# Kernel optimization log

Hardware: AMD Instinct MI355X
Metric: run time of the kernel (lower is better)

The kernel has to match this reference:

```python
import jax, jax.numpy as jnp
import numpy as np

G = 60            # 60x60 macroblock MV grid (960px / 16px blocks)
IMAGE_SIZE = 960.0
LN_EPS = 1e-5


def layer_norm(x, g, b):
    mu = jnp.mean(x, -1, keepdims=True)
    var = jnp.var(x, -1, keepdims=True)
    return (x - mu) / jnp.sqrt(var + LN_EPS) * g + b


def setup_inputs() -> dict:
    key = jax.random.key(0)
    ks = iter(jax.random.split(key, 40))
    nk = lambda: next(ks)
    N = 4096
    MVF, BED, H = 64, 32, 128
    D_IN = MVF + BED  # 96

    def lin(out_d, in_d):
        w = jax.random.normal(nk(), (out_d, in_d), jnp.float32) * np.float32(1.0 / np.sqrt(in_d))
        b = jnp.zeros((out_d,), jnp.float32)
        return w, b

    motion_vectors = jax.random.normal(nk(), (1, 2, G, G), jnp.float32)
    xy = jax.random.uniform(nk(), (N, 2), jnp.float32, 0.0, 800.0)
    wh = jax.random.uniform(nk(), (N, 2), jnp.float32, 16.0, 160.0)
    boxes = jnp.concatenate([xy, jnp.clip(xy + wh, 0.0, IMAGE_SIZE)], axis=-1)

    inp = {"motion_vectors": motion_vectors, "boxes": boxes}
    # stats projection: 6 stats (mean/std/range x 2 channels) -> MVF
    inp["W_stats"], inp["b_stats"] = lin(MVF, 6)
    inp["g_stats"] = jnp.ones((MVF,), jnp.float32); inp["be_stats"] = jnp.zeros((MVF,), jnp.float32)
    # box coordinate encoder
    inp["W_b1"], inp["b_b1"] = lin(BED, 4)
    inp["g_b1"] = jnp.ones((BED,), jnp.float32); inp["be_b1"] = jnp.zeros((BED,), jnp.float32)
    inp["W_b2"], inp["b_b2"] = lin(BED, BED)
    inp["g_b2"] = jnp.ones((BED,), jnp.float32); inp["be_b2"] = jnp.zeros((BED,), jnp.float32)
    # single-layer LSTM (torch gate order i,f,g,o)
    inp["W_ih"] = jax.random.normal(nk(), (4 * H, D_IN), jnp.float32) * np.float32(1.0 / np.sqrt(D_IN))
    inp["W_hh"] = jax.random.normal(nk(), (4 * H, H), jnp.float32) * np.float32(1.0 / np.sqrt(H))
    inp["b_ih"] = jnp.zeros((4 * H,), jnp.float32)
    inp["b_hh"] = jnp.zeros((4 * H,), jnp.float32)
    # heads
    inp["W_p1"], inp["b_p1"] = lin(H // 2, H); inp["W_p2"], inp["b_p2"] = lin(2, H // 2)
    inp["W_s1"], inp["b_s1"] = lin(H // 2, H); inp["W_s2"], inp["b_s2"] = lin(2, H // 2)
    inp["W_c1"], inp["b_c1"] = lin(H // 2, H); inp["W_c2"], inp["b_c2"] = lin(1, H // 2)
    return inp


def _box_motion_stats(motion_vectors, boxes_norm):
    # motion_vectors: [1,2,G,G]; boxes_norm: [N,4] in [0,1]
    mvf = motion_vectors[0].reshape(2, G * G)  # [2, 3600]
    x1 = jnp.clip(jnp.floor(boxes_norm[:, 0] * G).astype(jnp.int32), 0, G - 1)
    y1 = jnp.clip(jnp.floor(boxes_norm[:, 1] * G).astype(jnp.int32), 0, G - 1)
    x2 = jnp.clip(jnp.ceil(boxes_norm[:, 2] * G).astype(jnp.int32), x1 + 1, G)
    y2 = jnp.clip(jnp.ceil(boxes_norm[:, 3] * G).astype(jnp.int32), y1 + 1, G)
    idx = jnp.arange(G)
    mx = (idx[None, :] >= x1[:, None]) & (idx[None, :] < x2[:, None])  # [N,G]
    my = (idx[None, :] >= y1[:, None]) & (idx[None, :] < y2[:, None])  # [N,G]
    mask = (my[:, :, None] & mx[:, None, :]).reshape(-1, G * G).astype(mvf.dtype)  # [N,3600]
    cnt = mask.sum(-1, keepdims=True)  # >= 1 by construction
    s = jnp.einsum('nc,kc->nk', mask, mvf)          # [N,2]
    sq = jnp.einsum('nc,kc->nk', mask, mvf * mvf)   # [N,2]
    mean = s / cnt
    std = jnp.sqrt(jnp.clip(sq / cnt - mean * mean, 0.0))
    big = jnp.asarray(1e30, mvf.dtype)
    hi = jnp.where(mask[:, None, :] > 0, mvf[None], -big).max(-1)  # [N,2]
    lo = jnp.where(mask[:, None, :] > 0, mvf[None], big).min(-1)   # [N,2]
    return jnp.concatenate([mean, std, hi - lo], axis=-1)  # [N,6]


def reference(motion_vectors, boxes,
              W_stats, b_stats, g_stats, be_stats,
              W_b1, b_b1, g_b1, be_b1, W_b2, b_b2, g_b2, be_b2,
              W_ih, W_hh, b_ih, b_hh,
              W_p1, b_p1, W_p2, b_p2, W_s1, b_s1, W_s2, b_s2, W_c1, b_c1, W_c2, b_c2):
    N = boxes.shape[0]
    H = W_hh.shape[1]
    boxes_norm = jnp.clip(boxes / IMAGE_SIZE, 0.0, 1.0)

    # per-box motion feature (BoxAlignedMotionEncoder: gather region -> mean/std/range -> proj)
    stats = _box_motion_stats(motion_vectors, boxes_norm)
    mv_feat = jax.nn.relu(layer_norm(stats @ W_stats.T + b_stats, g_stats, be_stats))  # [N,64]

    # box coordinate encoder (dropout = identity in eval)
    h1 = jax.nn.relu(layer_norm(boxes_norm @ W_b1.T + b_b1, g_b1, be_b1))
    box_feat = jax.nn.relu(layer_norm(h1 @ W_b2.T + b_b2, g_b2, be_b2))  # [N,32]

    x = jnp.concatenate([mv_feat, box_feat], axis=-1)  # [N,96]

    # single-step LSTM, zero initial state, torch gate order i,f,g,o
    h0 = jnp.zeros((N, H), x.dtype)
    c0 = jnp.zeros((N, H), x.dtype)
    gates = x @ W_ih.T + h0 @ W_hh.T + b_ih + b_hh
    i, f, g, o = jnp.split(gates, 4, axis=-1)
    c = jax.nn.sigmoid(f) * c0 + jax.nn.sigmoid(i) * jnp.tanh(g)
    h = jax.nn.sigmoid(o) * jnp.tanh(c)  # [N,128]

    pos = jax.nn.relu(h @ W_p1.T + b_p1) @ W_p2.T + b_p2    # [N,2]
    size = jax.nn.relu(h @ W_s1.T + b_s1) @ W_s2.T + b_s2   # [N,2]
    conf = jax.nn.relu(h @ W_c1.T + b_c1) @ W_c2.T + b_c2   # [N,1]
    confidences = jax.nn.sigmoid(conf[:, 0])

    # box update: shift center by deltas, scale w/h by exp(size_deltas)
    x1, y1, x2, y2 = boxes[:, 0], boxes[:, 1], boxes[:, 2], boxes[:, 3]
    cx, cy = (x1 + x2) * 0.5, (y1 + y2) * 0.5
    w, hgt = x2 - x1, y2 - y1
    ncx, ncy = cx + pos[:, 0], cy + pos[:, 1]
    nw, nh = w * jnp.exp(size[:, 0]), hgt * jnp.exp(size[:, 1])
    pred = jnp.stack([ncx - nw * 0.5, ncy - nh * 0.5, ncx + nw * 0.5, ncy + nh * 0.5], axis=-1)
    return jnp.concatenate([pred, confidences[:, None]], axis=-1)  # [N,5]
```

## Files before the change

### kernel.cpp

```cpp
#include <hip/hip_runtime.h>
#include <math.h>

#define GRID_G 60
#define GRID_GG 3600
#define BPB 8

__device__ __forceinline__ float wred32sum(float v){
  #pragma unroll
  for (int m = 16; m; m >>= 1) v += __shfl_xor(v, m, 32);
  return v;
}
__device__ __forceinline__ float wred32max(float v){
  #pragma unroll
  for (int m = 16; m; m >>= 1) v = fmaxf(v, __shfl_xor(v, m, 32));
  return v;
}
__device__ __forceinline__ float wred32min(float v){
  #pragma unroll
  for (int m = 16; m; m >>= 1) v = fminf(v, __shfl_xor(v, m, 32));
  return v;
}
__device__ __forceinline__ float frcp(float x){ return __builtin_amdgcn_rcpf(x); }
__device__ __forceinline__ float fsig(float x){ return frcp(1.0f + __expf(-x)); }
__device__ __forceinline__ float ftanh(float x){ return 1.0f - 2.0f*frcp(1.0f + __expf(2.0f*x)); }

__device__ __forceinline__ unsigned short f2bf(float x){
  unsigned int u = __float_as_uint(x);
  return (unsigned short)((u + 0x7fffu + ((u >> 16) & 1u)) >> 16);
}
__device__ __forceinline__ float bf_lo(unsigned int u){ return __uint_as_float(u << 16); }
__device__ __forceinline__ float bf_hi(unsigned int u){ return __uint_as_float(u & 0xffff0000u); }

__global__ __launch_bounds__(256) void transpose_kernel(
    const float* __restrict__ W_ih,
    const float* __restrict__ W_p1, const float* __restrict__ W_s1,
    const float* __restrict__ W_c1,
    unsigned int* __restrict__ wt_ih2, unsigned int* __restrict__ wt_h2)
{
  const int i = blockIdx.x * 256 + threadIdx.x;
  if (i < 18432) {
    const int e = i * 2;
    const int k = e / 384, r0 = e % 384;
    const int row0 = (r0     < 128) ? r0     : r0 + 128;
    const int row1 = (r0 + 1 < 128) ? r0 + 1 : r0 + 1 + 128;
    const unsigned int lo = f2bf(W_ih[row0 * 96 + k]);
    const unsigned int hi = f2bf(W_ih[row1 * 96 + k]);
    wt_ih2[i] = lo | (hi << 16);
  } else if (i < 18432 + 12288) {
    const int j = i - 18432;
    const int e = j * 2;
    const int k = e / 192, r0 = e % 192;
    const float* W = (r0 < 64) ? W_p1 : (r0 < 128) ? W_s1 : W_c1;
    const unsigned int lo = f2bf(W[((r0    ) & 63) * 128 + k]);
    const unsigned int hi = f2bf(W[((r0 + 1) & 63) * 128 + k]);
    wt_h2[j] = lo | (hi << 16);
  }
}

__global__ __launch_bounds__(256) void tracker_kernel(
    const float* __restrict__ mv,
    const float* __restrict__ boxes,
    const float* __restrict__ W_stats, const float* __restrict__ b_stats,
    const float* __restrict__ g_stats, const float* __restrict__ be_stats,
    const float* __restrict__ W_b1,  const float* __restrict__ b_b1,
    const float* __restrict__ g_b1,  const float* __restrict__ be_b1,
    const float* __restrict__ W_b2,  const float* __restrict__ b_b2,
    const float* __restrict__ g_b2,  const float* __restrict__ be_b2,
    const unsigned int* __restrict__ wt_ih2,
    const float* __restrict__ b_ih,  const float* __restrict__ b_hh,
    const unsigned int* __restrict__ wt_h2,
    const float* __restrict__ b_p1,  const float* __restrict__ W_p2, const float* __restrict__ b_p2,
    const float* __restrict__ b_s1,  const float* __restrict__ W_s2, const float* __restrict__ b_s2,
    const float* __restrict__ b_c1,  const float* __restrict__ W_c2, const float* __restrict__ b_c2,
    float* __restrict__ out, int N)
{
  __shared__ __align__(16) float x_lds[BPB][96];
  __shared__ __align__(16) float sP[4][BPB][384];
  __shared__ __align__(16) float h_lds[BPB][128];
  __shared__ __align__(16) float h1_lds[BPB][32];
  __shared__ float u_lds[3*BPB][65];
  __shared__ float res_lds[BPB][5];

  const int tid  = threadIdx.x;
  const int base = blockIdx.x * BPB;

  {
    const int b   = tid >> 5;
    const int l32 = tid & 31;
    int gb = base + b; if (gb >= N) gb = N - 1;
    const float4 bx = ((const float4*)boxes)[gb];
    const float bn0 = fminf(fmaxf(bx.x * (1.0f/960.0f), 0.f), 1.f);
    const float bn1 = fminf(fmaxf(bx.y * (1.0f/960.0f), 0.f), 1.f);
    const float bn2 = fminf(fmaxf(bx.z * (1.0f/960.0f), 0.f), 1.f);
    const float bn3 = fminf(fmaxf(bx.w * (1.0f/960.0f), 0.f), 1.f);

    int x1 = (int)floorf(bn0 * 60.f); x1 = min(max(x1, 0), 59);
    int y1 = (int)floorf(bn1 * 60.f); y1 = min(max(y1, 0), 59);
    int x2 = (int)ceilf (bn2 * 60.f); x2 = min(max(x2, x1 + 1), 60);
    int y2 = (int)ceilf (bn3 * 60.f); y2 = min(max(y2, y1 + 1), 60);
    const int w = x2 - x1, hh = y2 - y1;
    const int cnt = w * hh;
    const float rw = 1.0f / (float)w;

    float s0=0.f, s1=0.f, q0=0.f, q1=0.f;
    float hi0=-1e30f, hi1=-1e30f, lo0=1e30f, lo1=1e30f;
    for (int c = l32; c < cnt; c += 32) {
      const int yy = (int)(((float)c + 0.5f) * rw);
      const int xx = c - yy * w;
      const int idx = (y1 + yy) * GRID_G + (x1 + xx);
      const float m0 = mv[idx];
      const float m1 = mv[GRID_GG + idx];
      s0 += m0; q0 += m0*m0; hi0 = fmaxf(hi0, m0); lo0 = fminf(lo0, m0);
      s1 += m1; q1 += m1*m1; hi1 = fmaxf(hi1, m1); lo1 = fminf(lo1, m1);
    }
    s0 = wred32sum(s0); q0 = wred32sum(q0); hi0 = wred32max(hi0); lo0 = wred32min(lo0);
    s1 = wred32sum(s1); q1 = wred32sum(q1); hi1 = wred32max(hi1); lo1 = wred32min(lo1);
    const float inv = frcp((float)cnt);
    float st[6];
    st[0] = s0 * inv;
    st[1] = s1 * inv;
    st[2] = sqrtf(fmaxf(q0 * inv - st[0]*st[0], 0.f));
    st[3] = sqrtf(fmaxf(q1 * inv - st[1]*st[1], 0.f));
    st[4] = hi0 - lo0;
    st[5] = hi1 - lo1;

    {
      const float* Wr0 = W_stats + l32 * 6;
      const float* Wr1 = W_stats + (l32 + 32) * 6;
      float v0 = b_stats[l32], v1 = b_stats[l32 + 32];
      #pragma unroll
      for (int k = 0; k < 6; ++k) { v0 = fmaf(st[k], Wr0[k], v0); v1 = fmaf(st[k], Wr1[k], v1); }
      const float mu  = wred32sum(v0 + v1) * (1.0f/64.0f);
      const float var = wred32sum(v0*v0 + v1*v1) * (1.0f/64.0f) - mu*mu;
      const float rs  = rsqrtf(var + 1e-5f);
      x_lds[b][l32     ] = fmaxf((v0-mu)*rs*g_stats[l32     ] + be_stats[l32     ], 0.f);
      x_lds[b][l32 + 32] = fmaxf((v1-mu)*rs*g_stats[l32 + 32] + be_stats[l32 + 32], 0.f);
    }

    {
      const float* Wr = W_b1 + l32 * 4;
      const float v = b_b1[l32] + bn0*Wr[0] + bn1*Wr[1] + bn2*Wr[2] + bn3*Wr[3];
      const float mu  = wred32sum(v)   * (1.0f/32.0f);
      const float var = wred32sum(v*v) * (1.0f/32.0f) - mu*mu;
      h1_lds[b][l32] = fmaxf((v - mu) * rsqrtf(var + 1e-5f) * g_b1[l32] + be_b1[l32], 0.f);
    }
    __threadfence_block();

    {
      const float* Wr = W_b2 + l32 * 32;
      float v = b_b2[l32];
      #pragma unroll
      for (int kk = 0; kk < 8; ++kk) {
        const float4 hv = *(const float4*)(&h1_lds[b][kk * 4]);
        const float4 wv = *(const float4*)(&Wr[kk * 4]);
        v = fmaf(wv.x,hv.x, fmaf(wv.y,hv.y, fmaf(wv.z,hv.z, fmaf(wv.w,hv.w, v))));
      }
      const float mu  = wred32sum(v)   * (1.0f/32.0f);
      const float var = wred32sum(v*v) * (1.0f/32.0f) - mu*mu;
      x_lds[b][64 + l32] = fmaxf((v - mu) * rsqrtf(var + 1e-5f) * g_b2[l32] + be_b2[l32], 0.f);
    }
  }
  __syncthreads();

  if (tid < 192) {
    const int o = tid % 48;
    const int s = tid / 48;
    const int k0 = s * 24;
    float acc[8][BPB];
    #pragma unroll
    for (int j = 0; j < 8; ++j)
      #pragma unroll
      for (int b = 0; b < BPB; ++b) acc[j][b] = 0.f;
    #pragma unroll 2
    for (int k4 = 0; k4 < 6; ++k4) {
      const int kb = k0 + 4*k4;
      uint4 W[4];
      #pragma unroll
      for (int kk = 0; kk < 4; ++kk)
        W[kk] = *(const uint4*)(wt_ih2 + ((size_t)(kb + kk) * 384 + 8*o) / 2);
      float4 xv[BPB];
      #pragma unroll
      for (int b = 0; b < BPB; ++b) xv[b] = *(const float4*)(&x_lds[b][kb]);
      #pragma unroll
      for (int kk = 0; kk < 4; ++kk) {
        const float w0 = bf_lo(W[kk].x), w1 = bf_hi(W[kk].x);
        const float w2 = bf_lo(W[kk].y), w3 = bf_hi(W[kk].y);
        const float w4 = bf_lo(W[kk].z), w5 = bf_hi(W[kk].z);
        const float w6 = bf_lo(W[kk].w), w7 = bf_hi(W[kk].w);
        #pragma unroll
        for (int b = 0; b < BPB; ++b) {
          const float xc = (kk == 0) ? xv[b].x : (kk == 1) ? xv[b].y : (kk == 2) ? xv[b].z : xv[b].w;
          acc[0][b] = fmaf(w0, xc, acc[0][b]);
          acc[1][b] = fmaf(w1, xc, acc[1][b]);
          acc[2][b] = fmaf(w2, xc, acc[2][b]);
          acc[3][b] = fmaf(w3, xc, acc[3][b]);
          acc[4][b] = fmaf(w4, xc, acc[4][b]);
          acc[5][b] = fmaf(w5, xc, acc[5][b]);
          acc[6][b] = fmaf(w6, xc, acc[6][b]);
          acc[7][b] = fmaf(w7, xc, acc[7][b]);
        }
      }
    }
    #pragma unroll
    for (int b = 0; b < BPB; ++b) {
      float4 v0; v0.x = acc[0][b]; v0.y = acc[1][b]; v0.z = acc[2][b]; v0.w = acc[3][b];
      float4 v1; v1.x = acc[4][b]; v1.y = acc[5][b]; v1.z = acc[6][b]; v1.w = acc[7][b];
      *(float4*)(&sP[s][b][8*o    ]) = v0;
      *(float4*)(&sP[s][b][8*o + 4]) = v1;
    }
  }
  __syncthreads();

  {
    const int j  = tid & 127;
    const int g2 = tid >> 7;
    const float bi = b_ih[j      ] + b_hh[j      ];
    const float bg = b_ih[j + 256] + b_hh[j + 256];
    const float bo = b_ih[j + 384] + b_hh[j + 384];
    #pragma unroll
    for (int bb = 0; bb < 4; ++bb) {
      const int b = g2 * 4 + bb;
      const float ai = sP[0][b][j      ] + sP[1][b][j      ] + sP[2][b][j      ] + sP[3][b][j      ] + bi;
      const float ag = sP[0][b][128 + j] + sP[1][b][128 + j] + sP[2][b][128 + j] + sP[3][b][128 + j] + bg;
      const float ao = sP[0][b][256 + j] + sP[1][b][256 + j] + sP[2][b][256 + j] + sP[3][b][256 + j] + bo;
      const float c  = fsig(ai) * ftanh(ag);
      h_lds[b][j] = fsig(ao) * ftanh(c);
    }
  }
  __syncthreads();

  if (tid < 192) {
    const int o  = tid % 24;
    const int s8 = tid / 24;
    const int k0 = s8 * 16;
    float acc[8][BPB];
    #pragma unroll
    for (int j = 0; j < 8; ++j)
      #pragma unroll
      for (int b = 0; b < BPB; ++b) acc[j][b] = 0.f;
    #pragma unroll 2
    for (int k4 = 0; k4 < 4; ++k4) {
      const int kb = k0 + 4*k4;
      uint4 W[4];
      #pragma unroll
      for (int kk = 0; kk < 4; ++kk)
        W[kk] = *(const uint4*)(wt_h2 + ((size_t)(kb + kk) * 192 + 8*o) / 2);
      float4 hv[BPB];
      #pragma unroll
      for (int b = 0; b < BPB; ++b) hv[b] = *(const float4*)(&h_lds[b][kb]);
      #pragma unroll
      for (int kk = 0; kk < 4; ++kk) {
        const float w0 = bf_lo(W[kk].x), w1 = bf_hi(W[kk].x);
        const float w2 = bf_lo(W[kk].y), w3 = bf_hi(W[kk].y);
        const float w4 = bf_lo(W[kk].z), w5 = bf_hi(W[kk].z);
        const float w6 = bf_lo(W[kk].w), w7 = bf_hi(W[kk].w);
        #pragma unroll
        for (int b = 0; b < BPB; ++b) {
          const float hc = (kk == 0) ? hv[b].x : (kk == 1) ? hv[b].y : (kk == 2) ? hv[b].z : hv[b].w;
          acc[0][b] = fmaf(w0, hc, acc[0][b]);
          acc[1][b] = fmaf(w1, hc, acc[1][b]);
          acc[2][b] = fmaf(w2, hc, acc[2][b]);
          acc[3][b] = fmaf(w3, hc, acc[3][b]);
          acc[4][b] = fmaf(w4, hc, acc[4][b]);
          acc[5][b] = fmaf(w5, hc, acc[5][b]);
          acc[6][b] = fmaf(w6, hc, acc[6][b]);
          acc[7][b] = fmaf(w7, hc, acc[7][b]);
        }
      }
    }
    const int buf = s8 >> 1;
    const int off = (s8 & 1) * 192;
    #pragma unroll
    for (int b = 0; b < BPB; ++b) {
      float4 v0; v0.x = acc[0][b]; v0.y = acc[1][b]; v0.z = acc[2][b]; v0.w = acc[3][b];
      float4 v1; v1.x = acc[4][b]; v1.y = acc[5][b]; v1.z = acc[6][b]; v1.w = acc[7][b];
      *(float4*)(&sP[buf][b][off + 8*o    ]) = v0;
      *(float4*)(&sP[buf][b][off + 8*o + 4]) = v1;
    }
  }
  __syncthreads();

  {
    #pragma unroll
    for (int i = 0; i < 6; ++i) {
      const int idx = tid + 256 * i;
      const int b = idx / 192;
      const int r = idx - b * 192;
      const int head = r >> 6, brow = r & 63;
      const float bias = ((head == 0) ? b_p1 : (head == 1) ? b_s1 : b_c1)[brow];
      float v = bias;
      #pragma unroll
      for (int p = 0; p < 8; ++p) v += sP[p >> 1][b][(p & 1) * 192 + r];
      u_lds[head * BPB + b][brow] = fmaxf(v, 0.f);
    }
  }
  __syncthreads();

  if (tid < BPB * 5) {
    const int b = tid / 5, o = tid % 5;
    const int head = (o < 2) ? 0 : (o < 4) ? 1 : 2;
    const float* W2; float bias;
    if      (o == 0) { W2 = W_p2;      bias = b_p2[0]; }
    else if (o == 1) { W2 = W_p2 + 64; bias = b_p2[1]; }
    else if (o == 2) { W2 = W_s2;      bias = b_s2[0]; }
    else if (o == 3) { W2 = W_s2 + 64; bias = b_s2[1]; }
    else             { W2 = W_c2;      bias = b_c2[0]; }
    const float* ur = u_lds[head * BPB + b];
    float a0 = bias, a1 = 0.f, a2 = 0.f, a3 = 0.f;
    #pragma unroll 4
    for (int k = 0; k < 64; k += 4) {
      a0 = fmaf(ur[k  ], W2[k  ], a0);
      a1 = fmaf(ur[k+1], W2[k+1], a1);
      a2 = fmaf(ur[k+2], W2[k+2], a2);
      a3 = fmaf(ur[k+3], W2[k+3], a3);
    }
    res_lds[b][o] = (a0 + a1) + (a2 + a3);
  }
  __syncthreads();

  if (tid < BPB) {
    const int gb = base + tid;
    if (gb < N) {
      const float4 bx = ((const float4*)boxes)[gb];
      const float cx = (bx.x + bx.z) * 0.5f;
      const float cy = (bx.y + bx.w) * 0.5f;
      const float w  = bx.z - bx.x;
      const float hh = bx.w - bx.y;
      const float ncx = cx + res_lds[tid][0];
      const float ncy = cy + res_lds[tid][1];
      const float nw  = w  * __expf(res_lds[tid][2]);
      const float nh  = hh * __expf(res_lds[tid][3]);
      const float cf  = fsig(res_lds[tid][4]);
      float* op = out + (size_t)gb * 5;
      op[0] = ncx - nw * 0.5f;
      op[1] = ncy - nh * 0.5f;
      op[2] = ncx + nw * 0.5f;
      op[3] = ncy + nh * 0.5f;
      op[4] = cf;
    }
  }
}

extern "C" void kernel_launch(void* const* d_in, const int* in_sizes, int n_in,
                              void* d_out, int out_size, void* d_ws, size_t ws_size,
                              hipStream_t stream) {
  (void)n_in; (void)out_size; (void)ws_size;
  const float* mv       = (const float*)d_in[0];
  const float* boxes    = (const float*)d_in[1];
  const float* W_stats  = (const float*)d_in[2];
  const float* b_stats  = (const float*)d_in[3];
  const float* g_stats  = (const float*)d_in[4];
  const float* be_stats = (const float*)d_in[5];
  const float* W_b1     = (const float*)d_in[6];
  const float* b_b1     = (const float*)d_in[7];
  const float* g_b1     = (const float*)d_in[8];
  const float* be_b1    = (const float*)d_in[9];
  const float* W_b2     = (const float*)d_in[10];
  const float* b_b2     = (const float*)d_in[11];
  const float* g_b2     = (const float*)d_in[12];
  const float* be_b2    = (const float*)d_in[13];
  const float* W_ih     = (const float*)d_in[14];
  const float* b_ih     = (const float*)d_in[16];
  const float* b_hh     = (const float*)d_in[17];
  const float* W_p1     = (const float*)d_in[18];
  const float* b_p1     = (const float*)d_in[19];
  const float* W_p2     = (const float*)d_in[20];
  const float* b_p2     = (const float*)d_in[21];
  const float* W_s1     = (const float*)d_in[22];
  const float* b_s1     = (const float*)d_in[23];
  const float* W_s2     = (const float*)d_in[24];
  const float* b_s2     = (const float*)d_in[25];
  const float* W_c1     = (const float*)d_in[26];
  const float* b_c1     = (const float*)d_in[27];
  const float* W_c2     = (const float*)d_in[28];
  const float* b_c2     = (const float*)d_in[29];

  unsigned int* wt_ih2 = (unsigned int*)d_ws;
  unsigned int* wt_h2  = wt_ih2 + 18432;

  transpose_kernel<<<120, 256, 0, stream>>>(W_ih, W_p1, W_s1, W_c1, wt_ih2, wt_h2);

  const int N = in_sizes[1] / 4;
  const int grid = (N + BPB - 1) / BPB;
  tracker_kernel<<<grid, 256, 0, stream>>>(
      mv, boxes,
      W_stats, b_stats, g_stats, be_stats,
      W_b1, b_b1, g_b1, be_b1,
      W_b2, b_b2, g_b2, be_b2,
      wt_ih2, b_ih, b_hh,
      wt_h2,
      b_p1, W_p2, b_p2,
      b_s1, W_s2, b_s2,
      b_c1, W_c2, b_c2,
      (float*)d_out, N);
}
```

Baseline: 132.7 us.

## Halve boxes per block, use full 64-lane waves, prefetch weight tiles

Boxes per block drop from 8 to 4, so each box gets a full 64-lane wavefront for the motion-stat gather and the stats projection. Reductions now span 64 lanes, and the 32-wide layer norms mask out the upper lanes. The first weight tile of each GEMM stage is prefetched into registers early, before the preceding phase, so its load latency overlaps other work. The grid doubles and weights are reloaded for every block, so per-box weight traffic roughly doubles, and the fully unrolled loops raise register pressure.

```diff
diff --git a/kernel.cpp b/kernel.cpp
--- a/kernel.cpp
+++ b/kernel.cpp
@@ -3,21 +3,21 @@
 
 #define GRID_G 60
 #define GRID_GG 3600
-#define BPB 8
-
-__device__ __forceinline__ float wred32sum(float v){
+#define BPB 4
+
+__device__ __forceinline__ float wredsum(float v){
   #pragma unroll
-  for (int m = 16; m; m >>= 1) v += __shfl_xor(v, m, 32);
+  for (int m = 32; m; m >>= 1) v += __shfl_xor(v, m, 64);
   return v;
 }
-__device__ __forceinline__ float wred32max(float v){
+__device__ __forceinline__ float wredmax(float v){
   #pragma unroll
-  for (int m = 16; m; m >>= 1) v = fmaxf(v, __shfl_xor(v, m, 32));
+  for (int m = 32; m; m >>= 1) v = fmaxf(v, __shfl_xor(v, m, 64));
   return v;
 }
-__device__ __forceinline__ float wred32min(float v){
+__device__ __forceinline__ float wredmin(float v){
   #pragma unroll
-  for (int m = 16; m; m >>= 1) v = fminf(v, __shfl_xor(v, m, 32));
+  for (int m = 32; m; m >>= 1) v = fminf(v, __shfl_xor(v, m, 64));
   return v;
 }
 __device__ __forceinline__ float frcp(float x){ return __builtin_amdgcn_rcpf(x); }
@@ -84,9 +84,20 @@
   const int tid  = threadIdx.x;
   const int base = blockIdx.x * BPB;
 
+  const int o2 = tid % 48, s2 = tid / 48;
+  const int o3 = tid % 24, s3 = tid / 24;
+  uint4 Wpre2[4];
+  if (tid < 192) {
+    const int k0 = s2 * 24;
+    #pragma unroll
+    for (int kk = 0; kk < 4; ++kk)
+      Wpre2[kk] = *(const uint4*)(wt_ih2 + ((size_t)(k0 + kk) * 384 + 8*o2) / 2);
+  }
+
   {
-    const int b   = tid >> 5;
-    const int l32 = tid & 31;
+    const int b    = tid >> 6;
+    const int lane = tid & 63;
+    const int l32  = lane & 31;
     int gb = base + b; if (gb >= N) gb = N - 1;
     const float4 bx = ((const float4*)boxes)[gb];
     const float bn0 = fminf(fmaxf(bx.x * (1.0f/960.0f), 0.f), 1.f);
@@ -104,7 +115,7 @@
 
     float s0=0.f, s1=0.f, q0=0.f, q1=0.f;
     float hi0=-1e30f, hi1=-1e30f, lo0=1e30f, lo1=1e30f;
-    for (int c = l32; c < cnt; c += 32) {
+    for (int c = lane; c < cnt; c += 64) {
       const int yy = (int)(((float)c + 0.5f) * rw);
       const int xx = c - yy * w;
       const int idx = (y1 + yy) * GRID_G + (x1 + xx);
@@ -113,8 +124,8 @@
       s0 += m0; q0 += m0*m0; hi0 = fmaxf(hi0, m0); lo0 = fminf(lo0, m0);
       s1 += m1; q1 += m1*m1; hi1 = fmaxf(hi1, m1); lo1 = fminf(lo1, m1);
     }
-    s0 = wred32sum(s0); q0 = wred32sum(q0); hi0 = wred32max(hi0); lo0 = wred32min(lo0);
-    s1 = wred32sum(s1); q1 = wred32sum(q1); hi1 = wred32max(hi1); lo1 = wred32min(lo1);
+    s0 = wredsum(s0); q0 = wredsum(q0); hi0 = wredmax(hi0); lo0 = wredmin(lo0);
+    s1 = wredsum(s1); q1 = wredsum(q1); hi1 = wredmax(hi1); lo1 = wredmin(lo1);
     const float inv = frcp((float)cnt);
     float st[6];
     st[0] = s0 * inv;
@@ -125,24 +136,24 @@
     st[5] = hi1 - lo1;
 
     {
-      const float* Wr0 = W_stats + l32 * 6;
-      const float* Wr1 = W_stats + (l32 + 32) * 6;
-      float v0 = b_stats[l32], v1 = b_stats[l32 + 32];
-      #pragma unroll
-      for (int k = 0; k < 6; ++k) { v0 = fmaf(st[k], Wr0[k], v0); v1 = fmaf(st[k], Wr1[k], v1); }
-      const float mu  = wred32sum(v0 + v1) * (1.0f/64.0f);
-      const float var = wred32sum(v0*v0 + v1*v1) * (1.0f/64.0f) - mu*mu;
-      const float rs  = rsqrtf(var + 1e-5f);
-      x_lds[b][l32     ] = fmaxf((v0-mu)*rs*g_stats[l32     ] + be_stats[l32     ], 0.f);
-      x_lds[b][l32 + 32] = fmaxf((v1-mu)*rs*g_stats[l32 + 32] + be_stats[l32 + 32], 0.f);
+      const float* Wr = W_stats + lane * 6;
+      float v = b_stats[lane];
+      #pragma unroll
+      for (int k = 0; k < 6; ++k) v = fmaf(st[k], Wr[k], v);
+      const float mu  = wredsum(v)   * (1.0f/64.0f);
+      const float var = wredsum(v*v) * (1.0f/64.0f) - mu*mu;
+      x_lds[b][lane] = fmaxf((v - mu) * rsqrtf(var + 1e-5f) * g_stats[lane] + be_stats[lane], 0.f);
     }
 
     {
       const float* Wr = W_b1 + l32 * 4;
       const float v = b_b1[l32] + bn0*Wr[0] + bn1*Wr[1] + bn2*Wr[2] + bn3*Wr[3];
-      const float mu  = wred32sum(v)   * (1.0f/32.0f);
-      const float var = wred32sum(v*v) * (1.0f/32.0f) - mu*mu;
-      h1_lds[b][l32] = fmaxf((v - mu) * rsqrtf(var + 1e-5f) * g_b1[l32] + be_b1[l32], 0.f);
+      const float cv  = (lane < 32) ? v   : 0.f;
+      const float cq  = (lane < 32) ? v*v : 0.f;
+      const float mu  = wredsum(cv) * (1.0f/32.0f);
+      const float var = wredsum(cq) * (1.0f/32.0f) - mu*mu;
+      const float h1v = fmaxf((v - mu) * rsqrtf(var + 1e-5f) * g_b1[l32] + be_b1[l32], 0.f);
+      if (lane < 32) h1_lds[b][l32] = h1v;
     }
     __threadfence_block();
 
@@ -155,29 +166,36 @@
         const float4 wv = *(const float4*)(&Wr[kk * 4]);
         v = fmaf(wv.x,hv.x, fmaf(wv.y,hv.y, fmaf(wv.z,hv.z, fmaf(wv.w,hv.w, v))));
       }
-      const float mu  = wred32sum(v)   * (1.0f/32.0f);
-      const float var = wred32sum(v*v) * (1.0f/32.0f) - mu*mu;
-      x_lds[b][64 + l32] = fmaxf((v - mu) * rsqrtf(var + 1e-5f) * g_b2[l32] + be_b2[l32], 0.f);
-    }
-  }
-  __syncthreads();
-
+      const float cv  = (lane < 32) ? v   : 0.f;
+      const float cq  = (lane < 32) ? v*v : 0.f;
+      const float mu  = wredsum(cv) * (1.0f/32.0f);
+      const float var = wredsum(cq) * (1.0f/32.0f) - mu*mu;
+      const float y = fmaxf((v - mu) * rsqrtf(var + 1e-5f) * g_b2[l32] + be_b2[l32], 0.f);
+      if (lane < 32) x_lds[b][64 + l32] = y;
+    }
+  }
+  __syncthreads();
+
+  uint4 Wpre3[4];
   if (tid < 192) {
-    const int o = tid % 48;
-    const int s = tid / 48;
-    const int k0 = s * 24;
+    const int k0 = s2 * 24;
     float acc[8][BPB];
     #pragma unroll
     for (int j = 0; j < 8; ++j)
       #pragma unroll
       for (int b = 0; b < BPB; ++b) acc[j][b] = 0.f;
-    #pragma unroll 2
+    #pragma unroll
     for (int k4 = 0; k4 < 6; ++k4) {
       const int kb = k0 + 4*k4;
       uint4 W[4];
-      #pragma unroll
-      for (int kk = 0; kk < 4; ++kk)
-        W[kk] = *(const uint4*)(wt_ih2 + ((size_t)(kb + kk) * 384 + 8*o) / 2);
+      if (k4 == 0) {
+        #pragma unroll
+        for (int kk = 0; kk < 4; ++kk) W[kk] = Wpre2[kk];
+      } else {
+        #pragma unroll
+        for (int kk = 0; kk < 4; ++kk)
+          W[kk] = *(const uint4*)(wt_ih2 + ((size_t)(kb + kk) * 384 + 8*o2) / 2);
+      }
       float4 xv[BPB];
       #pragma unroll
       for (int b = 0; b < BPB; ++b) xv[b] = *(const float4*)(&x_lds[b][kb]);
@@ -201,25 +219,31 @@
         }
       }
     }
+    {
+      const int k0h = s3 * 16;
+      #pragma unroll
+      for (int kk = 0; kk < 4; ++kk)
+        Wpre3[kk] = *(const uint4*)(wt_h2 + ((size_t)(k0h + kk) * 192 + 8*o3) / 2);
+    }
     #pragma unroll
     for (int b = 0; b < BPB; ++b) {
       float4 v0; v0.x = acc[0][b]; v0.y = acc[1][b]; v0.z = acc[2][b]; v0.w = acc[3][b];
       float4 v1; v1.x = acc[4][b]; v1.y = acc[5][b]; v1.z = acc[6][b]; v1.w = acc[7][b];
-      *(float4*)(&sP[s][b][8*o    ]) = v0;
-      *(float4*)(&sP[s][b][8*o + 4]) = v1;
+      *(float4*)(&sP[s2][b][8*o2    ]) = v0;
+      *(float4*)(&sP[s2][b][8*o2 + 4]) = v1;
     }
   }
   __syncthreads();
 
   {
-    const int j  = tid & 127;
-    const int g2 = tid >> 7;
+    const int j    = tid & 127;
+    const int half = tid >> 7;
     const float bi = b_ih[j      ] + b_hh[j      ];
     const float bg = b_ih[j + 256] + b_hh[j + 256];
     const float bo = b_ih[j + 384] + b_hh[j + 384];
     #pragma unroll
-    for (int bb = 0; bb < 4; ++bb) {
-      const int b = g2 * 4 + bb;
+    for (int bb = 0; bb < 2; ++bb) {
+      const int b = half * 2 + bb;
       const float ai = sP[0][b][j      ] + sP[1][b][j      ] + sP[2][b][j      ] + sP[3][b][j      ] + bi;
       const float ag = sP[0][b][128 + j] + sP[1][b][128 + j] + sP[2][b][128 + j] + sP[3][b][128 + j] + bg;
       const float ao = sP[0][b][256 + j] + sP[1][b][256 + j] + sP[2][b][256 + j] + sP[3][b][256 + j] + bo;
@@ -230,21 +254,24 @@
   __syncthreads();
 
   if (tid < 192) {
-    const int o  = tid % 24;
-    const int s8 = tid / 24;
-    const int k0 = s8 * 16;
+    const int k0 = s3 * 16;
     float acc[8][BPB];
     #pragma unroll
     for (int j = 0; j < 8; ++j)
       #pragma unroll
       for (int b = 0; b < BPB; ++b) acc[j][b] = 0.f;
-    #pragma unroll 2
+    #pragma unroll
     for (int k4 = 0; k4 < 4; ++k4) {
       const int kb = k0 + 4*k4;
       uint4 W[4];
-      #pragma unroll
-      for (int kk = 0; kk < 4; ++kk)
-        W[kk] = *(const uint4*)(wt_h2 + ((size_t)(kb + kk) * 192 + 8*o) / 2);
+      if (k4 == 0) {
+        #pragma unroll
+        for (int kk = 0; kk < 4; ++kk) W[kk] = Wpre3[kk];
+      } else {
+        #pragma unroll
+        for (int kk = 0; kk < 4; ++kk)
+          W[kk] = *(const uint4*)(wt_h2 + ((size_t)(kb + kk) * 192 + 8*o3) / 2);
+      }
       float4 hv[BPB];
       #pragma unroll
       for (int b = 0; b < BPB; ++b) hv[b] = *(const float4*)(&h_lds[b][kb]);
@@ -268,21 +295,21 @@
         }
       }
     }
-    const int buf = s8 >> 1;
-    const int off = (s8 & 1) * 192;
+    const int buf = s3 >> 1;
+    const int off = (s3 & 1) * 192;
     #pragma unroll
     for (int b = 0; b < BPB; ++b) {
       float4 v0; v0.x = acc[0][b]; v0.y = acc[1][b]; v0.z = acc[2][b]; v0.w = acc[3][b];
       float4 v1; v1.x = acc[4][b]; v1.y = acc[5][b]; v1.z = acc[6][b]; v1.w = acc[7][b];
-      *(float4*)(&sP[buf][b][off + 8*o    ]) = v0;
-      *(float4*)(&sP[buf][b][off + 8*o + 4]) = v1;
+      *(float4*)(&sP[buf][b][off + 8*o3    ]) = v0;
+      *(float4*)(&sP[buf][b][off + 8*o3 + 4]) = v1;
     }
   }
   __syncthreads();
 
   {
     #pragma unroll
-    for (int i = 0; i < 6; ++i) {
+    for (int i = 0; i < 3; ++i) {
       const int idx = tid + 256 * i;
       const int b = idx / 192;
       const int r = idx - b * 192;
```

Result: slower. 137.8 us (+3.9%).
